# Kernel tuning notes

Measured on AMD Instinct MI355X. Metric: run time of the kernel, lower is better.

Reference implementation:

```python
import jax, jax.numpy as jnp
import numpy as np

EPS = 1e-6

def _rmsnorm(x, w):
    return x * jax.lax.rsqrt(jnp.mean(x * x, axis=-1, keepdims=True) + EPS) * w

def _short_conv_silu(x, w):
    # x: [B,T,C], w: [C,K] depthwise causal conv then SiLU
    K = w.shape[1]
    T = x.shape[1]
    xp = jnp.pad(x, ((0, 0), (K - 1, 0), (0, 0)))
    y = sum(xp[:, i:i + T, :] * w[:, i] for i in range(K))
    return jax.nn.silu(y)

def _l2norm(x):
    return x * jax.lax.rsqrt(jnp.sum(x * x, axis=-1, keepdims=True) + EPS)

def setup_inputs():
    key = jax.random.key(0)
    ks = jax.random.split(key, 20)
    B, T, D = 4, 2048, 1024
    H, dk, dv = 8, 96, 192
    KD, VD, I = H * dk, H * dv, 4096
    s = 0.02
    r = lambda k, shp: jax.random.normal(k, shp, jnp.float32) * s
    return {
        "x": jax.random.normal(ks[0], (B, T, D), jnp.float32),
        "Wq": r(ks[1], (D, KD)),
        "Wk": r(ks[2], (D, KD)),
        "Wv": r(ks[3], (D, VD)),
        "Wb": r(ks[4], (D, H)),
        "Wa": r(ks[5], (D, H)),
        "A_log": jnp.log(jax.random.uniform(ks[6], (H,), jnp.float32, 1.0, 16.0)),
        "dt_bias": jax.random.normal(ks[7], (H,), jnp.float32) * 0.1,
        "conv_q_w": jax.random.normal(ks[8], (KD, 4), jnp.float32) * 0.2,
        "conv_k_w": jax.random.normal(ks[9], (KD, 4), jnp.float32) * 0.2,
        "conv_v_w": jax.random.normal(ks[10], (VD, 4), jnp.float32) * 0.2,
        "Wg": r(ks[11], (D, VD)),
        "onorm_w": jnp.ones((dv,), jnp.float32),
        "Wo": r(ks[12], (VD, D)),
        "norm1_w": jnp.ones((D,), jnp.float32),
        "norm2_w": jnp.ones((D,), jnp.float32),
        "Wgate": r(ks[13], (D, I)),
        "Wup": r(ks[14], (D, I)),
        "Wdown": r(ks[15], (I, D)),
    }

def reference(x, Wq, Wk, Wv, Wb, Wa, A_log, dt_bias, conv_q_w, conv_k_w, conv_v_w,
              Wg, onorm_w, Wo, norm1_w, norm2_w, Wgate, Wup, Wdown):
    B, T, D = x.shape
    H = A_log.shape[0]
    dk = Wq.shape[1] // H
    dv = Wv.shape[1] // H
    scale = dk ** -0.5

    # --- pre-norm + token mixer (GatedDeltaNet attention) ---
    h = _rmsnorm(x, norm1_w)
    q = _short_conv_silu(h @ Wq, conv_q_w).reshape(B, T, H, dk)
    k = _short_conv_silu(h @ Wk, conv_k_w).reshape(B, T, H, dk)
    v = _short_conv_silu(h @ Wv, conv_v_w).reshape(B, T, H, dv)
    q = _l2norm(q) * scale
    k = _l2norm(k)
    beta = jax.nn.sigmoid(h @ Wb)                               # [B,T,H]
    g = -jnp.exp(A_log) * jax.nn.softplus(h @ Wa + dt_bias)    # [B,T,H], <= 0

    # gated delta-rule recurrence: S_t = exp(g_t)*S_{t-1} + k_t (beta_t*(v_t - S^T k_t))^T
    def step(S, inp):
        q_t, k_t, v_t, g_t, b_t = inp
        S = S * jnp.exp(g_t)[..., None, None]
        v_old = jnp.einsum('bhk,bhkv->bhv', k_t, S)
        delta = (v_t - v_old) * b_t[..., None]
        S = S + jnp.einsum('bhk,bhv->bhkv', k_t, delta)
        o_t = jnp.einsum('bhk,bhkv->bhv', q_t, S)
        return S, o_t

    S0 = jnp.zeros((B, H, dk, dv), x.dtype)
    xs = (jnp.moveaxis(q, 1, 0), jnp.moveaxis(k, 1, 0), jnp.moveaxis(v, 1, 0),
          jnp.moveaxis(g, 1, 0), jnp.moveaxis(beta, 1, 0))
    _, o = jax.lax.scan(step, S0, xs)
    o = jnp.moveaxis(o, 0, 1)                                   # [B,T,H,dv]

    # gated RMSNorm output gate, then output projection
    g_out = (h @ Wg).reshape(B, T, H, dv)
    o = _rmsnorm(o, onorm_w) * jax.nn.silu(g_out)
    x = x + o.reshape(B, T, H * dv) @ Wo

    # --- pre-norm + SwiGLU MLP ---
    h2 = _rmsnorm(x, norm2_w)
    mlp = (jax.nn.silu(h2 @ Wgate) * (h2 @ Wup)) @ Wdown
    return x + mlp
```

## Files before the change

kernel.cpp:

```cpp
#include <hip/hip_runtime.h>
#include <hip/hip_bf16.h>

typedef __hip_bfloat16 bf16;
typedef unsigned short us;
typedef short short8v __attribute__((ext_vector_type(8)));
typedef float f32x4 __attribute__((ext_vector_type(4)));
typedef __attribute__((address_space(3))) unsigned int lds_u32;
typedef __attribute__((address_space(1))) const unsigned int glb_u32;

#define GLOAD16(gp, lp) __builtin_amdgcn_global_load_lds((glb_u32*)(gp), (lds_u32*)(lp), 16, 0, 0)

#define Bz 4
#define Tz 2048
#define Dz 1024
#define Hz 8
#define DKz 96
#define DVz 192
#define KDz 768
#define VDz 1536
#define Iz 4096
#define BTz (Bz*Tz)

static __device__ __forceinline__ float us2f(us s){
  return __uint_as_float(((unsigned)s) << 16);
}
static __device__ __forceinline__ us f2bs(float f){
  bf16 t = __float2bfloat16(f);
  return *(us*)&t;
}
static __device__ __forceinline__ float sigmoidf_(float x){ return 1.f/(1.f+expf(-x)); }
static __device__ __forceinline__ float siluf_(float x){ return x*sigmoidf_(x); }

#define DPPADD(x, ctrl) \
  ((x) + __int_as_float(__builtin_amdgcn_update_dpp(0, __float_as_int(x), (ctrl), 0xF, 0xF, true)))
static __device__ __forceinline__ float gsum16(float x){
  x = DPPADD(x, 0xB1);
  x = DPPADD(x, 0x4E);
  x = DPPADD(x, 0x141);
  x = DPPADD(x, 0x140);
  return x;
}

__global__ __launch_bounds__(256) void wprep_kernel(
    const float* __restrict__ Wsrc, us* __restrict__ WTdst, int K, int N)
{
  __shared__ float t[32][33];
  const int k0 = blockIdx.x*32, n0 = blockIdx.y*32;
  const int c = threadIdx.x & 31, r8 = threadIdx.x >> 5;
  #pragma unroll
  for (int i=0;i<4;i++){
    const int r = r8 + i*8;
    t[r][c] = Wsrc[(size_t)(k0+r)*N + n0 + c];
  }
  __syncthreads();
  #pragma unroll
  for (int i=0;i<4;i++){
    const int r = r8 + i*8;
    WTdst[(size_t)(n0+r)*K + k0 + c] = f2bs(t[c][r]);
  }
}

__global__ __launch_bounds__(256) void rmsnorm_kernel(
    const float* __restrict__ x, const float* __restrict__ w, bf16* __restrict__ out)
{
  const int row = blockIdx.x;
  const float* xr = x + (size_t)row*Dz;
  const int i0 = threadIdx.x*4;
  float4 xv = *(const float4*)(xr + i0);
  float ss = xv.x*xv.x+xv.y*xv.y+xv.z*xv.z+xv.w*xv.w;
  #pragma unroll
  for (int off=32; off>=1; off>>=1) ss += __shfl_xor(ss, off);
  __shared__ float red[4];
  if ((threadIdx.x&63)==0) red[threadIdx.x>>6] = ss;
  __syncthreads();
  ss = red[0]+red[1]+red[2]+red[3];
  const float inv = rsqrtf(ss*(1.f/Dz) + 1e-6f);
  float4 wv = *(const float4*)(w + i0);
  ushort4 ov;
  ov.x=f2bs(xv.x*inv*wv.x); ov.y=f2bs(xv.y*inv*wv.y);
  ov.z=f2bs(xv.z*inv*wv.z); ov.w=f2bs(xv.w*inv*wv.w);
  *(ushort4*)((us*)out + (size_t)row*Dz + i0) = ov;
}

template<int MODE>
__global__ __launch_bounds__(256, 2) void mgemm_kernel(
    const bf16* __restrict__ A, const us* __restrict__ BT,
    const void* __restrict__ res, void* __restrict__ Cout,
    int M, int N, int K)
{
  __shared__ us As[128*64];
  __shared__ us Bs[128*64];
  const int nwgx = gridDim.x;
  const int lid = blockIdx.y*nwgx + blockIdx.x;
  const int cpx = (nwgx*gridDim.y) >> 3;
  const int swz = (lid & 7)*cpx + (lid >> 3);
  const int m0 = (swz / nwgx)*128, n0 = (swz % nwgx)*128;
  const int tid = threadIdx.x;
  const int wid = tid >> 6, lane = tid & 63;
  const int wr = wid >> 1, wc = wid & 1;
  const int fq = lane >> 4, fr = lane & 15;

  const us* Ab = (const us*)A + (size_t)(m0 + (tid>>3))*K + (tid&7)*8;
  const us* Bb = BT + (size_t)(n0 + (tid>>3))*K + (tid&7)*8;
  char* AsB = (char*)As;
  char* BsB = (char*)Bs;
  const int ldsoff = wid*1024;

  f32x4 acc[4][4] = {};
  const int nk = K >> 6;
  for (int kt = 0; kt < nk; ++kt){
    const int kb = kt*64;
    #pragma unroll
    for (int i=0;i<4;i++){
      GLOAD16(Ab + (size_t)(32*i)*K + kb, AsB + ldsoff + i*4096);
      GLOAD16(Bb + (size_t)(32*i)*K + kb, BsB + ldsoff + i*4096);
    }
    __syncthreads();
    #pragma unroll
    for (int ks=0; ks<2; ks++){
      short8v af[4], bf[4];
      #pragma unroll
      for (int r=0;r<4;r++)
        af[r] = *(const short8v*)&As[(wr*64 + r*16 + fr)*64 + ks*32 + fq*8];
      #pragma unroll
      for (int c=0;c<4;c++)
        bf[c] = *(const short8v*)&Bs[(wc*64 + c*16 + fr)*64 + ks*32 + fq*8];
      #pragma unroll
      for (int r=0;r<4;r++)
        #pragma unroll
        for (int c=0;c<4;c++)
          acc[r][c] = __builtin_amdgcn_mfma_f32_16x16x32_bf16(af[r], bf[c], acc[r][c], 0, 0, 0);
    }
    __syncthreads();
  }
  #pragma unroll
  for (int r=0;r<4;r++){
    #pragma unroll
    for (int c=0;c<4;c++){
      const int col = n0 + wc*64 + c*16 + fr;
      #pragma unroll
      for (int jj=0;jj<4;jj++){
        const int row = m0 + wr*64 + r*16 + fq*4 + jj;
        const size_t idx = (size_t)row*N + col;
        const float a = acc[r][c][jj];
        if (MODE==0){
          ((us*)Cout)[idx] = f2bs(a);
        } else if (MODE==1){
          ((float*)Cout)[idx] = a + ((const float*)res)[idx];
        } else {
          ((us*)Cout)[idx] = f2bs(siluf_(us2f(((const us*)res)[idx]))*a);
        }
      }
    }
  }
}

__global__ __launch_bounds__(256) void beta_g_kernel(
    const bf16* __restrict__ hh, const float* __restrict__ Wb, const float* __restrict__ Wa,
    const float* __restrict__ A_log, const float* __restrict__ dt_bias,
    float2* __restrict__ meta)
{
  const int row = blockIdx.x;
  const us* hr = (const us*)hh + (size_t)row*Dz;
  float ab[8]={0,0,0,0,0,0,0,0}, aa[8]={0,0,0,0,0,0,0,0};
  for (int kk=threadIdx.x; kk<Dz; kk+=256){
    const float hv = us2f(hr[kk]);
    float4 b0 = *(const float4*)(Wb + kk*8);
    float4 b1 = *(const float4*)(Wb + kk*8 + 4);
    float4 a0 = *(const float4*)(Wa + kk*8);
    float4 a1 = *(const float4*)(Wa + kk*8 + 4);
    ab[0]=fmaf(hv,b0.x,ab[0]); ab[1]=fmaf(hv,b0.y,ab[1]);
    ab[2]=fmaf(hv,b0.z,ab[2]); ab[3]=fmaf(hv,b0.w,ab[3]);
    ab[4]=fmaf(hv,b1.x,ab[4]); ab[5]=fmaf(hv,b1.y,ab[5]);
    ab[6]=fmaf(hv,b1.z,ab[6]); ab[7]=fmaf(hv,b1.w,ab[7]);
    aa[0]=fmaf(hv,a0.x,aa[0]); aa[1]=fmaf(hv,a0.y,aa[1]);
    aa[2]=fmaf(hv,a0.z,aa[2]); aa[3]=fmaf(hv,a0.w,aa[3]);
    aa[4]=fmaf(hv,a1.x,aa[4]); aa[5]=fmaf(hv,a1.y,aa[5]);
    aa[6]=fmaf(hv,a1.z,aa[6]); aa[7]=fmaf(hv,a1.w,aa[7]);
  }
  #pragma unroll
  for (int off=32; off>=1; off>>=1){
    #pragma unroll
    for (int n=0;n<8;n++){ ab[n]+=__shfl_xor(ab[n],off); aa[n]+=__shfl_xor(aa[n],off); }
  }
  __shared__ float red[4][16];
  const int wv = threadIdx.x>>6, ln = threadIdx.x&63;
  if (ln==0){
    #pragma unroll
    for (int n=0;n<8;n++){ red[wv][n]=ab[n]; red[wv][8+n]=aa[n]; }
  }
  __syncthreads();
  if (threadIdx.x < 8){
    const int n = threadIdx.x;
    float sb = red[0][n]+red[1][n]+red[2][n]+red[3][n];
    float sa = red[0][8+n]+red[1][8+n]+red[2][8+n]+red[3][8+n];
    float xx = sa + dt_bias[n];
    float sp = (xx > 20.f) ? xx : log1pf(expf(xx));
    float eg = expf(-expf(A_log[n])*sp);
    float bt = 1.f/(1.f+expf(-sb));
    meta[(size_t)row*Hz + n] = make_float2(eg, bt);
  }
}

__global__ __launch_bounds__(64) void conv_kq_kernel(
    const bf16* __restrict__ preq, const bf16* __restrict__ prek,
    const float* __restrict__ wqc, const float* __restrict__ wkc,
    us* __restrict__ kqn)
{
  const int idx = blockIdx.x; const int h = idx & 7; const int bt = idx >> 3;
  const int t = bt & (Tz-1);
  const int lane = threadIdx.x;
  const us* Q = (const us*)preq;
  const us* K = (const us*)prek;
  const int c0 = h*DKz + lane, c1 = c0 + 64;
  const bool hi = lane < 32;
  float yq0=0.f, yq1=0.f, yk0=0.f, yk1=0.f;
  #pragma unroll
  for (int i=0;i<4;i++){
    const int ti = t - 3 + i;
    if (ti >= 0){
      const size_t rowb = (size_t)(bt-3+i)*KDz;
      yq0 = fmaf(us2f(Q[rowb + c0]), wqc[c0*4+i], yq0);
      yk0 = fmaf(us2f(K[rowb + c0]), wkc[c0*4+i], yk0);
      if (hi){
        yq1 = fmaf(us2f(Q[rowb + c1]), wqc[c1*4+i], yq1);
        yk1 = fmaf(us2f(K[rowb + c1]), wkc[c1*4+i], yk1);
      }
    }
  }
  yq0 = siluf_(yq0); yk0 = siluf_(yk0);
  yq1 = hi ? siluf_(yq1) : 0.f;
  yk1 = hi ? siluf_(yk1) : 0.f;
  float ssq = yq0*yq0 + yq1*yq1;
  float ssk = yk0*yk0 + yk1*yk1;
  #pragma unroll
  for (int off=32; off>=1; off>>=1){ ssq += __shfl_xor(ssq,off); ssk += __shfl_xor(ssk,off); }
  const float iq = rsqrtf(ssq + 1e-6f) * 0.10206207262f;
  const float ik = rsqrtf(ssk + 1e-6f);
  const size_t base = (size_t)bt*1536 + (size_t)h*192;
  kqn[base + lane]      = f2bs(yk0*ik);
  kqn[base + 96 + lane] = f2bs(yq0*iq);
  if (hi){
    kqn[base + 64 + lane]      = f2bs(yk1*ik);
    kqn[base + 96 + 64 + lane] = f2bs(yq1*iq);
  }
}

__global__ __launch_bounds__(256) void conv_apply_v_kernel(
    const bf16* __restrict__ prev, const float* __restrict__ wvc, bf16* __restrict__ vn)
{
  const int bt = blockIdx.y; const int ccol = blockIdx.x*256 + threadIdx.x;
  const int t = bt & (Tz-1);
  const us* X = (const us*)prev;
  float acc = 0.f;
  #pragma unroll
  for (int i=0;i<4;i++){
    const int ti = t - 3 + i;
    if (ti >= 0) acc = fmaf(us2f(X[(size_t)(bt-3+i)*VDz + ccol]), wvc[ccol*4+i], acc);
  }
  ((us*)vn)[(size_t)bt*VDz + ccol] = f2bs(siluf_(acc));
}

__global__ __launch_bounds__(192, 1) void scan_kernel(
    const us* __restrict__ kqn, const bf16* __restrict__ vn,
    const float2* __restrict__ meta, bf16* __restrict__ o)
{
  const int blk = blockIdx.x;
  const int bh = blk >> 4, sp = blk & 15;
  const int b = bh >> 3, h = bh & 7;
  const int tid = threadIdx.x;
  const int g = tid & 15;
  const int j = tid >> 4;
  const int vc = h*DVz + sp*12 + j;

  __shared__ float kq[2][8][192];

  const us* KQ = kqn + (size_t)b*Tz*1536 + h*192 + tid;
  const us* VP = (const us*)vn + (size_t)b*Tz*VDz + vc;
  us* op = (us*)o + (size_t)b*Tz*VDz + vc;
  const float2* MP = meta + (size_t)b*Tz*Hz + h;

  float S[6];
  #pragma unroll
  for (int m=0;m<6;m++) S[m]=0.f;

  float ced[8], egb[8], cvb[8];

  #pragma unroll
  for (int s=0;s<8;s++){
    kq[0][s][tid] = us2f(KQ[(size_t)s*1536]);
    const float cv = us2f(VP[(size_t)s*VDz]);
    const float2 m = MP[(size_t)s*Hz];
    ced[s] = m.x; egb[s] = m.x*m.y; cvb[s] = cv*m.y;
  }
  __syncthreads();

  for (int ph=0; ph<Tz/8; ph++){
    const int base = ph*8;
    const int p = ph & 1;
    const bool more = (base + 8 < Tz);
    const int nb = more ? base + 8 : base;
    float nkq[8], nv[8]; float2 nm[8];
    #pragma unroll
    for (int s=0;s<8;s++){
      nkq[s] = us2f(KQ[(size_t)(nb+s)*1536]);
      nv[s]  = us2f(VP[(size_t)(nb+s)*VDz]);
      nm[s]  = MP[(size_t)(nb+s)*Hz];
    }
    float2 kf[2][3], qf[2][3];
    #pragma unroll
    for (int m=0;m<3;m++){
      kf[0][m] = *(const float2*)&kq[p][0][g*6 + m*2];
      qf[0][m] = *(const float2*)&kq[p][0][96 + g*6 + m*2];
    }
    #pragma unroll
    for (int s=0;s<8;s++){
      const int cu = s & 1, nx = cu ^ 1;
      if (s < 7){
        #pragma unroll
        for (int m=0;m<3;m++){
          kf[nx][m] = *(const float2*)&kq[p][s+1][g*6 + m*2];
          qf[nx][m] = *(const float2*)&kq[p][s+1][96 + g*6 + m*2];
        }
      }
      float a0, a1;
      a0 = kf[cu][0].x*S[0];          a1 = kf[cu][0].y*S[1];
      a0 = fmaf(kf[cu][1].x,S[2],a0); a1 = fmaf(kf[cu][1].y,S[3],a1);
      a0 = fmaf(kf[cu][2].x,S[4],a0); a1 = fmaf(kf[cu][2].y,S[5],a1);
      const float pv = gsum16(a0+a1);
      const float eg = ced[s];
      const float delta = fmaf(-egb[s], pv, cvb[s]);
      float o0, o1, t0;
      t0 = fmaf(eg,S[0], kf[cu][0].x*delta); S[0]=t0; o0 = qf[cu][0].x*t0;
      t0 = fmaf(eg,S[1], kf[cu][0].y*delta); S[1]=t0; o1 = qf[cu][0].y*t0;
      t0 = fmaf(eg,S[2], kf[cu][1].x*delta); S[2]=t0; o0 = fmaf(qf[cu][1].x,t0,o0);
      t0 = fmaf(eg,S[3], kf[cu][1].y*delta); S[3]=t0; o1 = fmaf(qf[cu][1].y,t0,o1);
      t0 = fmaf(eg,S[4], kf[cu][2].x*delta); S[4]=t0; o0 = fmaf(qf[cu][2].x,t0,o0);
      t0 = fmaf(eg,S[5], kf[cu][2].y*delta); S[5]=t0; o1 = fmaf(qf[cu][2].y,t0,o1);
      const float po = gsum16(o0+o1);
      if (g == 0) op[(size_t)(base+s)*VDz] = f2bs(po);
    }
    if (more){
      #pragma unroll
      for (int s=0;s<8;s++){
        kq[p^1][s][tid] = nkq[s];
        ced[s] = nm[s].x; egb[s] = nm[s].x*nm[s].y; cvb[s] = nv[s]*nm[s].y;
      }
    }
    __syncthreads();
  }
}

__global__ __launch_bounds__(64) void gate_out_kernel(
    const bf16* __restrict__ o, const bf16* __restrict__ gout,
    const float* __restrict__ onw, bf16* __restrict__ og)
{
  const size_t base = (size_t)blockIdx.x * DVz;
  const int lane = threadIdx.x;
  const us* O = (const us*)o;
  float x0 = us2f(O[base+lane]), x1 = us2f(O[base+64+lane]), x2 = us2f(O[base+128+lane]);
  float ss = x0*x0 + x1*x1 + x2*x2;
  #pragma unroll
  for (int off=32; off>=1; off>>=1) ss += __shfl_xor(ss, off);
  const float inv = rsqrtf(ss*(1.f/DVz) + 1e-6f);
  const us* G = (const us*)gout;
  us* OG = (us*)og;
  float xs[3] = {x0, x1, x2};
  #pragma unroll
  for (int i=0;i<3;i++){
    const int c = lane + 64*i;
    const float gv = us2f(G[base+c]);
    OG[base+c] = f2bs(xs[i]*inv*onw[c] * siluf_(gv));
  }
}

extern "C" void kernel_launch(void* const* d_in, const int* in_sizes, int n_in,
                              void* d_out, int out_size, void* d_ws, size_t ws_size,
                              hipStream_t stream) {
  const float* x        = (const float*)d_in[0];
  const float* Wq       = (const float*)d_in[1];
  const float* Wk       = (const float*)d_in[2];
  const float* Wv       = (const float*)d_in[3];
  const float* Wb       = (const float*)d_in[4];
  const float* Wa       = (const float*)d_in[5];
  const float* A_log    = (const float*)d_in[6];
  const float* dt_bias  = (const float*)d_in[7];
  const float* conv_q_w = (const float*)d_in[8];
  const float* conv_k_w = (const float*)d_in[9];
  const float* conv_v_w = (const float*)d_in[10];
  const float* Wg       = (const float*)d_in[11];
  const float* onorm_w  = (const float*)d_in[12];
  const float* Wo       = (const float*)d_in[13];
  const float* norm1_w  = (const float*)d_in[14];
  const float* norm2_w  = (const float*)d_in[15];
  const float* Wgate    = (const float*)d_in[16];
  const float* Wup      = (const float*)d_in[17];
  const float* Wdown    = (const float*)d_in[18];

  char* W = (char*)d_ws;
  us* WoT    = (us*)(W + 0);
  us* WgateT = (us*)(W + 3145728);
  us* WupT   = (us*)(W + 11534336);
  us* WdownT = (us*)(W + 19922944);
  us* WqT    = (us*)(W + 28311552);
  us* WkT    = (us*)(W + 29884416);
  us* WvT    = (us*)(W + 31457280);
  us* WgT    = (us*)(W + 34603008);
  bf16*   h_   = (bf16*)  (W + 37748736);
  bf16*   preq = (bf16*)  (W + 54525952);
  bf16*   prek = (bf16*)  (W + 67108864);
  bf16*   prev = (bf16*)  (W + 79691776);
  float2* meta = (float2*)(W + 104857600);
  bf16*   gout = (bf16*)  (W + 105906176);
  us*    kqn   = (us*)   (W + 28311552);
  bf16*  vn    = (bf16*) (W + 54525952);
  bf16*  o_    = (bf16*) (W + 79691776);
  bf16*  og    = (bf16*) (W + 28311552);
  float* x2    = (float*)(W + 79691776);
  bf16*  h2    = (bf16*) (W + 113246208);
  bf16*  gateC = (bf16*) (W + 28311552);

  wprep_kernel<<<dim3(48,32),  256, 0, stream>>>(Wo,    WoT,    1536, 1024);
  wprep_kernel<<<dim3(32,128), 256, 0, stream>>>(Wgate, WgateT, 1024, 4096);
  wprep_kernel<<<dim3(32,128), 256, 0, stream>>>(Wup,   WupT,   1024, 4096);
  wprep_kernel<<<dim3(128,32), 256, 0, stream>>>(Wdown, WdownT, 4096, 1024);
  wprep_kernel<<<dim3(32,24),  256, 0, stream>>>(Wq,    WqT,    1024, 768);
  wprep_kernel<<<dim3(32,24),  256, 0, stream>>>(Wk,    WkT,    1024, 768);
  wprep_kernel<<<dim3(32,48),  256, 0, stream>>>(Wv,    WvT,    1024, 1536);
  wprep_kernel<<<dim3(32,48),  256, 0, stream>>>(Wg,    WgT,    1024, 1536);
  rmsnorm_kernel<<<BTz, 256, 0, stream>>>(x, norm1_w, h_);
  mgemm_kernel<0><<<dim3(6,64),  256, 0, stream>>>(h_, WqT, nullptr, preq, BTz, KDz, Dz);
  mgemm_kernel<0><<<dim3(6,64),  256, 0, stream>>>(h_, WkT, nullptr, prek, BTz, KDz, Dz);
  mgemm_kernel<0><<<dim3(12,64), 256, 0, stream>>>(h_, WvT, nullptr, prev, BTz, VDz, Dz);
  beta_g_kernel<<<BTz, 256, 0, stream>>>(h_, Wb, Wa, A_log, dt_bias, meta);
  mgemm_kernel<0><<<dim3(12,64), 256, 0, stream>>>(h_, WgT, nullptr, gout, BTz, VDz, Dz);
  conv_kq_kernel<<<BTz*Hz, 64, 0, stream>>>(preq, prek, conv_q_w, conv_k_w, kqn);
  conv_apply_v_kernel<<<dim3(6, BTz), 256, 0, stream>>>(prev, conv_v_w, vn);
  scan_kernel<<<Bz*Hz*16, 192, 0, stream>>>(kqn, vn, meta, o_);
  gate_out_kernel<<<BTz*Hz, 64, 0, stream>>>(o_, gout, onorm_w, og);
  mgemm_kernel<1><<<dim3(8,64), 256, 0, stream>>>(og, WoT, x, x2, BTz, Dz, VDz);
  rmsnorm_kernel<<<BTz, 256, 0, stream>>>(x2, norm2_w, h2);
  for (int c = 0; c < 2; c++){
    const bf16*  h2c = h2 + (size_t)c*4096*Dz;
    const float* x2c = x2 + (size_t)c*4096*Dz;
    float*       out = (float*)d_out + (size_t)c*4096*Dz;
    mgemm_kernel<0><<<dim3(32,32), 256, 0, stream>>>(h2c, WgateT, nullptr, gateC, 4096, Iz, Dz);
    mgemm_kernel<3><<<dim3(32,32), 256, 0, stream>>>(h2c, WupT, gateC, gateC, 4096, Iz, Dz);
    mgemm_kernel<1><<<dim3(8,32),  256, 0, stream>>>(gateC, WdownT, x2c, out, 4096, Dz, Iz);
  }
}
```

Before: 1.228 ms.

## Split scan state across 32 lanes per value column and double block count

```diff
diff --git a/kernel.cpp b/kernel.cpp
--- a/kernel.cpp
+++ b/kernel.cpp
@@ -5,6 +5,7 @@
 typedef unsigned short us;
 typedef short short8v __attribute__((ext_vector_type(8)));
 typedef float f32x4 __attribute__((ext_vector_type(4)));
+typedef int int2v __attribute__((ext_vector_type(2)));
 typedef __attribute__((address_space(3))) unsigned int lds_u32;
 typedef __attribute__((address_space(1))) const unsigned int glb_u32;
 
@@ -33,12 +34,18 @@
 
 #define DPPADD(x, ctrl) \
   ((x) + __int_as_float(__builtin_amdgcn_update_dpp(0, __float_as_int(x), (ctrl), 0xF, 0xF, true)))
-static __device__ __forceinline__ float gsum16(float x){
+
+static __device__ __forceinline__ float gsum32(float x){
   x = DPPADD(x, 0xB1);
   x = DPPADD(x, 0x4E);
   x = DPPADD(x, 0x141);
   x = DPPADD(x, 0x140);
-  return x;
+#if __has_builtin(__builtin_amdgcn_permlane32_swap)
+  int2v r = __builtin_amdgcn_permlane32_swap(__float_as_int(x), __float_as_int(x), false, false);
+  return __int_as_float(r.x) + __int_as_float(r.y);
+#else
+  return x + __shfl_xor(x, 32);
+#endif
 }
 
 __global__ __launch_bounds__(256) void wprep_kernel(
@@ -261,34 +268,35 @@
   ((us*)vn)[(size_t)bt*VDz + ccol] = f2bs(siluf_(acc));
 }
 
-__global__ __launch_bounds__(192, 1) void scan_kernel(
+__global__ __launch_bounds__(192, 3) void scan_kernel(
     const us* __restrict__ kqn, const bf16* __restrict__ vn,
     const float2* __restrict__ meta, bf16* __restrict__ o)
 {
   const int blk = blockIdx.x;
-  const int bh = blk >> 4, sp = blk & 15;
+  const int bh = blk >> 5, sp = blk & 31;
   const int b = bh >> 3, h = bh & 7;
   const int tid = threadIdx.x;
-  const int g = tid & 15;
-  const int j = tid >> 4;
-  const int vc = h*DVz + sp*12 + j;
+  const int l = tid & 63, w = tid >> 6;
+  const int jloc = (l >> 4) & 1;
+  const int g = (l & 15) | ((l >> 5) << 4);
+  const int vc = h*DVz + sp*6 + 2*w + jloc;
 
   __shared__ float kq[2][8][192];
+
+  const int ch = (tid < 96) ? tid : (tid - 96);
+  const int spos = ((tid < 96) ? 0 : 96) + (ch % 3)*32 + (ch / 3);
 
   const us* KQ = kqn + (size_t)b*Tz*1536 + h*192 + tid;
   const us* VP = (const us*)vn + (size_t)b*Tz*VDz + vc;
   us* op = (us*)o + (size_t)b*Tz*VDz + vc;
   const float2* MP = meta + (size_t)b*Tz*Hz + h;
 
-  float S[6];
-  #pragma unroll
-  for (int m=0;m<6;m++) S[m]=0.f;
-
+  float S0=0.f, S1=0.f, S2=0.f;
   float ced[8], egb[8], cvb[8];
 
   #pragma unroll
   for (int s=0;s<8;s++){
-    kq[0][s][tid] = us2f(KQ[(size_t)s*1536]);
+    kq[0][s][spos] = us2f(KQ[(size_t)s*1536]);
     const float cv = us2f(VP[(size_t)s*VDz]);
     const float2 m = MP[(size_t)s*Hz];
     ced[s] = m.x; egb[s] = m.x*m.y; cvb[s] = cv*m.y;
@@ -307,43 +315,33 @@
       nv[s]  = us2f(VP[(size_t)(nb+s)*VDz]);
       nm[s]  = MP[(size_t)(nb+s)*Hz];
     }
-    float2 kf[2][3], qf[2][3];
-    #pragma unroll
-    for (int m=0;m<3;m++){
-      kf[0][m] = *(const float2*)&kq[p][0][g*6 + m*2];
-      qf[0][m] = *(const float2*)&kq[p][0][96 + g*6 + m*2];
-    }
+    float k0c[2], k1c[2], k2c[2], q0c[2], q1c[2], q2c[2];
+    k0c[0] = kq[p][0][g];      k1c[0] = kq[p][0][32+g];    k2c[0] = kq[p][0][64+g];
+    q0c[0] = kq[p][0][96+g];   q1c[0] = kq[p][0][128+g];   q2c[0] = kq[p][0][160+g];
     #pragma unroll
     for (int s=0;s<8;s++){
       const int cu = s & 1, nx = cu ^ 1;
       if (s < 7){
-        #pragma unroll
-        for (int m=0;m<3;m++){
-          kf[nx][m] = *(const float2*)&kq[p][s+1][g*6 + m*2];
-          qf[nx][m] = *(const float2*)&kq[p][s+1][96 + g*6 + m*2];
-        }
+        k0c[nx] = kq[p][s+1][g];     k1c[nx] = kq[p][s+1][32+g];  k2c[nx] = kq[p][s+1][64+g];
+        q0c[nx] = kq[p][s+1][96+g];  q1c[nx] = kq[p][s+1][128+g]; q2c[nx] = kq[p][s+1][160+g];
       }
-      float a0, a1;
-      a0 = kf[cu][0].x*S[0];          a1 = kf[cu][0].y*S[1];
-      a0 = fmaf(kf[cu][1].x,S[2],a0); a1 = fmaf(kf[cu][1].y,S[3],a1);
-      a0 = fmaf(kf[cu][2].x,S[4],a0); a1 = fmaf(kf[cu][2].y,S[5],a1);
-      const float pv = gsum16(a0+a1);
+      float a0 = k0c[cu]*S0;
+      a0 = fmaf(k1c[cu], S1, a0);
+      a0 = fmaf(k2c[cu], S2, a0);
+      const float pv = gsum32(a0);
       const float eg = ced[s];
       const float delta = fmaf(-egb[s], pv, cvb[s]);
-      float o0, o1, t0;
-      t0 = fmaf(eg,S[0], kf[cu][0].x*delta); S[0]=t0; o0 = qf[cu][0].x*t0;
-      t0 = fmaf(eg,S[1], kf[cu][0].y*delta); S[1]=t0; o1 = qf[cu][0].y*t0;
-      t0 = fmaf(eg,S[2], kf[cu][1].x*delta); S[2]=t0; o0 = fmaf(qf[cu][1].x,t0,o0);
-      t0 = fmaf(eg,S[3], kf[cu][1].y*delta); S[3]=t0; o1 = fmaf(qf[cu][1].y,t0,o1);
-      t0 = fmaf(eg,S[4], kf[cu][2].x*delta); S[4]=t0; o0 = fmaf(qf[cu][2].x,t0,o0);
-      t0 = fmaf(eg,S[5], kf[cu][2].y*delta); S[5]=t0; o1 = fmaf(qf[cu][2].y,t0,o1);
-      const float po = gsum16(o0+o1);
+      float t0, o0;
+      t0 = fmaf(eg, S0, k0c[cu]*delta); S0 = t0; o0 = q0c[cu]*t0;
+      t0 = fmaf(eg, S1, k1c[cu]*delta); S1 = t0; o0 = fmaf(q1c[cu], t0, o0);
+      t0 = fmaf(eg, S2, k2c[cu]*delta); S2 = t0; o0 = fmaf(q2c[cu], t0, o0);
+      const float po = gsum32(o0);
       if (g == 0) op[(size_t)(base+s)*VDz] = f2bs(po);
     }
     if (more){
       #pragma unroll
       for (int s=0;s<8;s++){
-        kq[p^1][s][tid] = nkq[s];
+        kq[p^1][s][spos] = nkq[s];
         ced[s] = nm[s].x; egb[s] = nm[s].x*nm[s].y; cvb[s] = nv[s]*nm[s].y;
       }
     }
@@ -436,7 +434,7 @@
   mgemm_kernel<0><<<dim3(12,64), 256, 0, stream>>>(h_, WgT, nullptr, gout, BTz, VDz, Dz);
   conv_kq_kernel<<<BTz*Hz, 64, 0, stream>>>(preq, prek, conv_q_w, conv_k_w, kqn);
   conv_apply_v_kernel<<<dim3(6, BTz), 256, 0, stream>>>(prev, conv_v_w, vn);
-  scan_kernel<<<Bz*Hz*16, 192, 0, stream>>>(kqn, vn, meta, o_);
+  scan_kernel<<<Bz*Hz*32, 192, 0, stream>>>(kqn, vn, meta, o_);
   gate_out_kernel<<<BTz*Hz, 64, 0, stream>>>(o_, gout, onorm_w, og);
   mgemm_kernel<1><<<dim3(8,64), 256, 0, stream>>>(og, WoT, x, x2, BTz, Dz, VDz);
   rmsnorm_kernel<<<BTz, 256, 0, stream>>>(x2, norm2_w, h2);
```

Result: slower. 1.356 ms (+10.4%).

## Fuse QKVG projections into one GEMM and gate/up into a dual GEMM

Applied to the files above, without the earlier changes.

```diff
diff --git a/kernel.cpp b/kernel.cpp
--- a/kernel.cpp
+++ b/kernel.cpp
@@ -145,11 +145,151 @@
         const float a = acc[r][c][jj];
         if (MODE==0){
           ((us*)Cout)[idx] = f2bs(a);
-        } else if (MODE==1){
+        } else {
           ((float*)Cout)[idx] = a + ((const float*)res)[idx];
-        } else {
-          ((us*)Cout)[idx] = f2bs(siluf_(us2f(((const us*)res)[idx]))*a);
         }
+      }
+    }
+  }
+}
+
+__global__ __launch_bounds__(256, 2) void proj_gemm_kernel(
+    const bf16* __restrict__ A, const us* __restrict__ BT,
+    us* __restrict__ preq, us* __restrict__ prek,
+    us* __restrict__ prev, us* __restrict__ gout,
+    int M, int N, int K)
+{
+  __shared__ us As[128*64];
+  __shared__ us Bs[128*64];
+  const int nwgx = gridDim.x;
+  const int lid = blockIdx.y*nwgx + blockIdx.x;
+  const int cpx = (nwgx*gridDim.y) >> 3;
+  const int swz = (lid & 7)*cpx + (lid >> 3);
+  const int m0 = (swz / nwgx)*128, n0 = (swz % nwgx)*128;
+  const int tid = threadIdx.x;
+  const int wid = tid >> 6, lane = tid & 63;
+  const int wr = wid >> 1, wc = wid & 1;
+  const int fq = lane >> 4, fr = lane & 15;
+
+  const us* Ab = (const us*)A + (size_t)(m0 + (tid>>3))*K + (tid&7)*8;
+  const us* Bb = BT + (size_t)(n0 + (tid>>3))*K + (tid&7)*8;
+  char* AsB = (char*)As;
+  char* BsB = (char*)Bs;
+  const int ldsoff = wid*1024;
+
+  f32x4 acc[4][4] = {};
+  const int nk = K >> 6;
+  for (int kt = 0; kt < nk; ++kt){
+    const int kb = kt*64;
+    #pragma unroll
+    for (int i=0;i<4;i++){
+      GLOAD16(Ab + (size_t)(32*i)*K + kb, AsB + ldsoff + i*4096);
+      GLOAD16(Bb + (size_t)(32*i)*K + kb, BsB + ldsoff + i*4096);
+    }
+    __syncthreads();
+    #pragma unroll
+    for (int ks=0; ks<2; ks++){
+      short8v af[4], bf[4];
+      #pragma unroll
+      for (int r=0;r<4;r++)
+        af[r] = *(const short8v*)&As[(wr*64 + r*16 + fr)*64 + ks*32 + fq*8];
+      #pragma unroll
+      for (int c=0;c<4;c++)
+        bf[c] = *(const short8v*)&Bs[(wc*64 + c*16 + fr)*64 + ks*32 + fq*8];
+      #pragma unroll
+      for (int r=0;r<4;r++)
+        #pragma unroll
+        for (int c=0;c<4;c++)
+          acc[r][c] = __builtin_amdgcn_mfma_f32_16x16x32_bf16(af[r], bf[c], acc[r][c], 0, 0, 0);
+    }
+    __syncthreads();
+  }
+  us* dst; int col0, Nout;
+  if (n0 < 768)      { dst = preq; col0 = n0;        Nout = 768;  }
+  else if (n0 < 1536){ dst = prek; col0 = n0 - 768;  Nout = 768;  }
+  else if (n0 < 3072){ dst = prev; col0 = n0 - 1536; Nout = 1536; }
+  else               { dst = gout; col0 = n0 - 3072; Nout = 1536; }
+  #pragma unroll
+  for (int r=0;r<4;r++){
+    #pragma unroll
+    for (int c=0;c<4;c++){
+      const int col = col0 + wc*64 + c*16 + fr;
+      #pragma unroll
+      for (int jj=0;jj<4;jj++){
+        const int row = m0 + wr*64 + r*16 + fq*4 + jj;
+        dst[(size_t)row*Nout + col] = f2bs(acc[r][c][jj]);
+      }
+    }
+  }
+}
+
+__global__ __launch_bounds__(256, 2) void mgemm_dual_kernel(
+    const bf16* __restrict__ A, const us* __restrict__ BT1, const us* __restrict__ BT2,
+    us* __restrict__ Cout, int M, int N, int K)
+{
+  __shared__ us As[128*64];
+  __shared__ us Bs1[128*64];
+  __shared__ us Bs2[128*64];
+  const int nwgx = gridDim.x;
+  const int lid = blockIdx.y*nwgx + blockIdx.x;
+  const int cpx = (nwgx*gridDim.y) >> 3;
+  const int swz = (lid & 7)*cpx + (lid >> 3);
+  const int m0 = (swz / nwgx)*128, n0 = (swz % nwgx)*128;
+  const int tid = threadIdx.x;
+  const int wid = tid >> 6, lane = tid & 63;
+  const int wr = wid >> 1, wc = wid & 1;
+  const int fq = lane >> 4, fr = lane & 15;
+
+  const us* Ab  = (const us*)A + (size_t)(m0 + (tid>>3))*K + (tid&7)*8;
+  const us* Bb1 = BT1 + (size_t)(n0 + (tid>>3))*K + (tid&7)*8;
+  const us* Bb2 = BT2 + (size_t)(n0 + (tid>>3))*K + (tid&7)*8;
+  char* AsB  = (char*)As;
+  char* BsB1 = (char*)Bs1;
+  char* BsB2 = (char*)Bs2;
+  const int ldsoff = wid*1024;
+
+  f32x4 acc1[4][4] = {};
+  f32x4 acc2[4][4] = {};
+  const int nk = K >> 6;
+  for (int kt = 0; kt < nk; ++kt){
+    const int kb = kt*64;
+    #pragma unroll
+    for (int i=0;i<4;i++){
+      GLOAD16(Ab  + (size_t)(32*i)*K + kb, AsB  + ldsoff + i*4096);
+      GLOAD16(Bb1 + (size_t)(32*i)*K + kb, BsB1 + ldsoff + i*4096);
+      GLOAD16(Bb2 + (size_t)(32*i)*K + kb, BsB2 + ldsoff + i*4096);
+    }
+    __syncthreads();
+    #pragma unroll
+    for (int ks=0; ks<2; ks++){
+      short8v af[4], bf1[4], bf2[4];
+      #pragma unroll
+      for (int r=0;r<4;r++)
+        af[r] = *(const short8v*)&As[(wr*64 + r*16 + fr)*64 + ks*32 + fq*8];
+      #pragma unroll
+      for (int c=0;c<4;c++){
+        bf1[c] = *(const short8v*)&Bs1[(wc*64 + c*16 + fr)*64 + ks*32 + fq*8];
+        bf2[c] = *(const short8v*)&Bs2[(wc*64 + c*16 + fr)*64 + ks*32 + fq*8];
+      }
+      #pragma unroll
+      for (int r=0;r<4;r++)
+        #pragma unroll
+        for (int c=0;c<4;c++){
+          acc1[r][c] = __builtin_amdgcn_mfma_f32_16x16x32_bf16(af[r], bf1[c], acc1[r][c], 0, 0, 0);
+          acc2[r][c] = __builtin_amdgcn_mfma_f32_16x16x32_bf16(af[r], bf2[c], acc2[r][c], 0, 0, 0);
+        }
+    }
+    __syncthreads();
+  }
+  #pragma unroll
+  for (int r=0;r<4;r++){
+    #pragma unroll
+    for (int c=0;c<4;c++){
+      const int col = n0 + wc*64 + c*16 + fr;
+      #pragma unroll
+      for (int jj=0;jj<4;jj++){
+        const int row = m0 + wr*64 + r*16 + fq*4 + jj;
+        Cout[(size_t)row*N + col] = f2bs(siluf_(acc1[r][c][jj]) * acc2[r][c][jj]);
       }
     }
   }
@@ -402,10 +542,7 @@
   us* WgateT = (us*)(W + 3145728);
   us* WupT   = (us*)(W + 11534336);
   us* WdownT = (us*)(W + 19922944);
-  us* WqT    = (us*)(W + 28311552);
-  us* WkT    = (us*)(W + 29884416);
-  us* WvT    = (us*)(W + 31457280);
-  us* WgT    = (us*)(W + 34603008);
+  us* WqkvgT = (us*)(W + 28311552);
   bf16*   h_   = (bf16*)  (W + 37748736);
   bf16*   preq = (bf16*)  (W + 54525952);
   bf16*   prek = (bf16*)  (W + 67108864);
@@ -415,8 +552,8 @@
   us*    kqn   = (us*)   (W + 28311552);
   bf16*  vn    = (bf16*) (W + 54525952);
   bf16*  o_    = (bf16*) (W + 79691776);
+  float* x2    = (float*)(W + 79691776);
   bf16*  og    = (bf16*) (W + 28311552);
-  float* x2    = (float*)(W + 79691776);
   bf16*  h2    = (bf16*) (W + 113246208);
   bf16*  gateC = (bf16*) (W + 28311552);
 
@@ -424,16 +561,14 @@
   wprep_kernel<<<dim3(32,128), 256, 0, stream>>>(Wgate, WgateT, 1024, 4096);
   wprep_kernel<<<dim3(32,128), 256, 0, stream>>>(Wup,   WupT,   1024, 4096);
   wprep_kernel<<<dim3(128,32), 256, 0, stream>>>(Wdown, WdownT, 4096, 1024);
-  wprep_kernel<<<dim3(32,24),  256, 0, stream>>>(Wq,    WqT,    1024, 768);
-  wprep_kernel<<<dim3(32,24),  256, 0, stream>>>(Wk,    WkT,    1024, 768);
-  wprep_kernel<<<dim3(32,48),  256, 0, stream>>>(Wv,    WvT,    1024, 1536);
-  wprep_kernel<<<dim3(32,48),  256, 0, stream>>>(Wg,    WgT,    1024, 1536);
+  wprep_kernel<<<dim3(32,24),  256, 0, stream>>>(Wq,    WqkvgT,             1024, 768);
+  wprep_kernel<<<dim3(32,24),  256, 0, stream>>>(Wk,    WqkvgT +  768*1024, 1024, 768);
+  wprep_kernel<<<dim3(32,48),  256, 0, stream>>>(Wv,    WqkvgT + 1536*1024, 1024, 1536);
+  wprep_kernel<<<dim3(32,48),  256, 0, stream>>>(Wg,    WqkvgT + 3072*1024, 1024, 1536);
   rmsnorm_kernel<<<BTz, 256, 0, stream>>>(x, norm1_w, h_);
-  mgemm_kernel<0><<<dim3(6,64),  256, 0, stream>>>(h_, WqT, nullptr, preq, BTz, KDz, Dz);
-  mgemm_kernel<0><<<dim3(6,64),  256, 0, stream>>>(h_, WkT, nullptr, prek, BTz, KDz, Dz);
-  mgemm_kernel<0><<<dim3(12,64), 256, 0, stream>>>(h_, WvT, nullptr, prev, BTz, VDz, Dz);
+  proj_gemm_kernel<<<dim3(36,64), 256, 0, stream>>>(h_, WqkvgT,
+      (us*)preq, (us*)prek, (us*)prev, (us*)gout, BTz, 4608, Dz);
   beta_g_kernel<<<BTz, 256, 0, stream>>>(h_, Wb, Wa, A_log, dt_bias, meta);
-  mgemm_kernel<0><<<dim3(12,64), 256, 0, stream>>>(h_, WgT, nullptr, gout, BTz, VDz, Dz);
   conv_kq_kernel<<<BTz*Hz, 64, 0, stream>>>(preq, prek, conv_q_w, conv_k_w, kqn);
   conv_apply_v_kernel<<<dim3(6, BTz), 256, 0, stream>>>(prev, conv_v_w, vn);
   scan_kernel<<<Bz*Hz*16, 192, 0, stream>>>(kqn, vn, meta, o_);
@@ -444,8 +579,8 @@
     const bf16*  h2c = h2 + (size_t)c*4096*Dz;
     const float* x2c = x2 + (size_t)c*4096*Dz;
     float*       out = (float*)d_out + (size_t)c*4096*Dz;
-    mgemm_kernel<0><<<dim3(32,32), 256, 0, stream>>>(h2c, WgateT, nullptr, gateC, 4096, Iz, Dz);
-    mgemm_kernel<3><<<dim3(32,32), 256, 0, stream>>>(h2c, WupT, gateC, gateC, 4096, Iz, Dz);
+    mgemm_dual_kernel<<<dim3(32,32), 256, 0, stream>>>(h2c, WgateT, WupT, (us*)gateC,
+                                                       4096, Iz, Dz);
     mgemm_kernel<1><<<dim3(8,32),  256, 0, stream>>>(gateC, WdownT, x2c, out, 4096, Dz, Iz);
   }
 }
```

Result: faster. 1.152 ms (-6.1%).
